# Kernel optimization log

Hardware: AMD Instinct MI355X
Metric: run time of the kernel (lower is better)

Reference implementation:

```python
import jax, jax.numpy as jnp
import numpy as np
from jax import lax

MAX_LEN = 50
MIN_LEN = 5
S = 2 * MAX_LEN + 1  # 101 states (2 branches)
NEG = -10000.0       # score for disallowed transitions


def _build_constraints():
    """Replicates CRFBaseModel.get_crf_constraints(max_len=50, min_len=5, n_branches=2)."""
    pairs = [(0, 0), (0, 1), (MAX_LEN, 1), (MAX_LEN, 0)]
    for i in range(1, MAX_LEN):
        pairs.append((i, i + 1))
        if i > MIN_LEN - 1:
            pairs.append((MIN_LEN - 2, i))
    pairs.append((MAX_LEN - 1, MAX_LEN))
    pairs.append((MAX_LEN - 1, MAX_LEN - 1))
    start_b = 1 + MAX_LEN
    end_b = 2 * MAX_LEN
    pairs += [(0, start_b), (end_b, start_b), (end_b, 0), (end_b, 1), (start_b - 1, start_b)]
    for i in range(start_b, end_b):
        pairs.append((i, i + 1))
        if i > MIN_LEN - 1:
            pairs.append((start_b + MIN_LEN - 3, i))
    pairs.append((end_b - 1, end_b - 1))
    allowed_t = np.zeros((S, S), dtype=bool)
    for (a, c) in pairs:
        allowed_t[a, c] = True
    allowed_s = np.zeros((S,), dtype=bool)
    allowed_s[[0, 1, start_b]] = True
    allowed_e = np.zeros((S,), dtype=bool)
    allowed_e[[0, MAX_LEN, end_b]] = True
    return allowed_t, allowed_s, allowed_e

_ALLOWED_T, _ALLOWED_S, _ALLOWED_E = _build_constraints()


def setup_inputs() -> dict:
    key = jax.random.key(0)
    k0, k1, k2, k3, k4 = jax.random.split(key, 5)
    B, T = 128, 2048
    features = jax.random.normal(k0, (B, T, 64), dtype=jnp.float32)
    mask = jnp.ones((B, T), dtype=bool)
    W = jax.random.normal(k1, (64, 3), dtype=jnp.float32) * 0.05
    b = jnp.zeros((3,), dtype=jnp.float32)
    start_transitions = jax.random.uniform(k2, (S,), minval=-0.1, maxval=0.1, dtype=jnp.float32)
    transitions = jax.random.uniform(k3, (S, S), minval=-0.1, maxval=0.1, dtype=jnp.float32)
    end_transitions = jax.random.uniform(k4, (S,), minval=-0.1, maxval=0.1, dtype=jnp.float32)
    return {"features": features, "mask": mask, "W": W, "b": b,
            "start_transitions": start_transitions, "transitions": transitions,
            "end_transitions": end_transitions}


def reference(features, mask, W, b, start_transitions, transitions, end_transitions):
    B, T, _ = features.shape
    # Apply hand-crafted transition constraints (disallowed -> -10000).
    trans = jnp.where(jnp.asarray(_ALLOWED_T), transitions, NEG)       # [S,S]
    start = jnp.where(jnp.asarray(_ALLOWED_S), start_transitions, NEG)  # [S]
    end = jnp.where(jnp.asarray(_ALLOWED_E), end_transitions, NEG)      # [S]

    # Emissions: linear head to 3 labels, repeated over the state space.
    e3 = features @ W + b  # [B,T,3]
    em = jnp.concatenate([
        e3[..., 0:1],
        jnp.broadcast_to(e3[..., 1:2], (B, T, MAX_LEN)),
        jnp.broadcast_to(e3[..., 2:3], (B, T, MAX_LEN)),
    ], axis=-1)  # [B,T,S]

    eT = jnp.moveaxis(em, 1, 0)    # [T,B,S]
    mT = jnp.moveaxis(mask, 1, 0)  # [T,B]

    # ---- forward (alpha) recursion ----
    a0 = start[None, :] + eT[0]  # [B,S]

    def fwd_step(a, inp):
        e_t, m_t = inp
        a_new = jax.nn.logsumexp(a[:, :, None] + trans[None], axis=1) + e_t
        a = jnp.where(m_t[:, None], a_new, a)
        return a, a

    _, alphas = lax.scan(fwd_step, a0, (eT[1:], mT[1:]))
    alpha = jnp.concatenate([a0[None], alphas], axis=0)  # [T,B,S]
    logZ = jax.nn.logsumexp(alpha[-1] + end[None, :], axis=-1)  # [B]

    # ---- backward (beta) recursion ----
    bT = jnp.broadcast_to(end[None, :], (B, S))

    def bwd_step(b_nxt, inp):
        e_nxt, m_nxt = inp
        b_new = jax.nn.logsumexp(trans[None] + (e_nxt + b_nxt)[:, None, :], axis=2)
        b_nxt = jnp.where(m_nxt[:, None], b_new, b_nxt)
        return b_nxt, b_nxt

    _, betas = lax.scan(bwd_step, bT, (eT[1:], mT[1:]), reverse=True)
    beta = jnp.concatenate([betas, bT[None]], axis=0)  # [T,B,S]

    # marginal probabilities p_t(s) = exp(alpha+beta-logZ) == softmax over states
    probs = jnp.moveaxis(jax.nn.softmax(alpha + beta, axis=-1), 0, 1)  # [B,T,S]

    # ---- Viterbi decode (top_k=1) ----
    def vit_step(v, inp):
        e_t, m_t = inp
        scores = v[:, :, None] + trans[None]   # [B,S_prev,S_cur]
        best = scores.max(axis=1)
        idx = scores.argmax(axis=1).astype(jnp.int32)
        v = jnp.where(m_t[:, None], best + e_t, v)
        return v, idx

    v_last, hist = lax.scan(vit_step, a0, (eT[1:], mT[1:]))  # hist: [T-1,B,S]
    final = v_last + end[None, :]
    last_state = jnp.argmax(final, axis=-1).astype(jnp.int32)  # [B]
    best_score = final.max(axis=-1)

    def back(state, h_t):
        prev = jnp.take_along_axis(h_t, state[:, None], axis=1)[:, 0]
        return prev, prev

    _, prevs = lax.scan(back, last_state, hist, reverse=True)  # [T-1,B]
    paths = jnp.concatenate([prevs, last_state[None]], axis=0).T  # [B,T]
    path_probs = jnp.exp(best_score - logZ)  # [B]
    return probs, paths, path_probs
```

## Files before the change

kernel.cpp:

```cpp
#include <hip/hip_runtime.h>
#include <hip/hip_bf16.h>
#include <math.h>

#define Tn 2048
#define Bn 128
#define Sn 101
#define HP 112
#define CL 128
#define NC (Tn / CL)
#define SEG 256
#define KSEG 8
#define SEGA 128
#define KA 16
#define WWA 128
#define WWARMV 512
#define NEGV -10000.0f
#define DIS  -3.0e38f
#define NINF2 -1.0e30f
#define L2E  1.442695041f

__device__ __forceinline__ int state_label(int s) { return (s == 0) ? 0 : ((s <= 50) ? 1 : 2); }

__device__ __forceinline__ float rl(float v, int lane) {
    return __int_as_float(__builtin_amdgcn_readlane(__float_as_int(v), lane));
}
__device__ __forceinline__ float slog2(float x) {
    return (x > 0.f) ? __log2f(x) : NINF2;
}

__device__ __forceinline__ float dpp_shr1(float x) {
    int xi = __float_as_int(x);
    return __int_as_float(__builtin_amdgcn_update_dpp(xi, xi, 0x138, 0xf, 0xf, false));
}
__device__ __forceinline__ float dpp_shl1(float x) {
    int xi = __float_as_int(x);
    return __int_as_float(__builtin_amdgcn_update_dpp(xi, xi, 0x130, 0xf, 0xf, false));
}
__device__ __forceinline__ float dpp_sum63(float x) {
    x += __int_as_float(__builtin_amdgcn_update_dpp(0, __float_as_int(x), 0x111, 0xf, 0xf, false));
    x += __int_as_float(__builtin_amdgcn_update_dpp(0, __float_as_int(x), 0x112, 0xf, 0xf, false));
    x += __int_as_float(__builtin_amdgcn_update_dpp(0, __float_as_int(x), 0x114, 0xf, 0xf, false));
    x += __int_as_float(__builtin_amdgcn_update_dpp(0, __float_as_int(x), 0x118, 0xf, 0xf, false));
    x += __int_as_float(__builtin_amdgcn_update_dpp(0, __float_as_int(x), 0x142, 0xf, 0xf, false));
    x += __int_as_float(__builtin_amdgcn_update_dpp(0, __float_as_int(x), 0x143, 0xf, 0xf, false));
    return x;
}
__device__ __forceinline__ float dpp_max63(float x) {
// ... 49 lines not shown
    float yA = eA * bA, yB = eB * bB;
    float yAdn = dpp_shl1(yA);
    float y0 = rl(yA, 0), y1 = rl(yB, 0), y51 = rl(yB, 25);
    float c3 = w3A * yA + w3B * yB;
    float c53 = w53A * yA + w53B * yB;
    float s3 = rl(dpp_sum63(c3), 63);
    float s53 = rl(dpp_sum63(c53), 63);
    float chA = (l == 50) ? y51 : yB;
    float nA = wAc * chA + wAs * yA + wA2 * y0 + wA3 * ((l == 0) ? y51 : y1);
    float nB = wBc * yAdn + wBs * yB;
    nB = (l == 1) ? s3 : ((l == 26) ? s53 : nB);
    bA = nA; bB = nB;
}

__global__ __launch_bounds__(256) void k_emis(const float* __restrict__ feat,
                                              const float* __restrict__ W,
                                              const float* __restrict__ bb,
                                              float* __restrict__ e3) {
    int row = blockIdx.x * 256 + threadIdx.x;
    if (row >= Bn * Tn) return;
    const float* f = feat + (size_t)row * 64;
    double a0 = 0.0, a1 = 0.0, a2 = 0.0;
    for (int i = 0; i < 64; i++) {
        double fv = (double)f[i];
        a0 += fv * (double)W[i * 3 + 0];
        a1 += fv * (double)W[i * 3 + 1];
        a2 += fv * (double)W[i * 3 + 2];
    }
    e3[(size_t)row * 3 + 0] = (float)(a0 + (double)bb[0]);
    e3[(size_t)row * 3 + 1] = (float)(a1 + (double)bb[1]);
    e3[(size_t)row * 3 + 2] = (float)(a2 + (double)bb[2]);
}

__global__ __launch_bounds__(64) void k1(const float* __restrict__ e3,
                                         const float* __restrict__ trans,
                                         const float* __restrict__ startT,
                                         const float* __restrict__ endT,
                                         float* __restrict__ alphaOut,
                                         float* __restrict__ shf,
                                         unsigned char* __restrict__ hist,
                                         float* __restrict__ wA,
                                         float* __restrict__ outLast,
                                         float* __restrict__ LSEend,
                                         float* __restrict__ vW,
                                         float* __restrict__ vOut,
                                         float* __restrict__ best,
                                         int* __restrict__ last,
                                         float* __restrict__ bhand)
{
    const int bid = blockIdx.x;
    const int l = threadIdx.x;
    const int sA = 2 * l, sB = 2 * l + 1;
    const bool hA = sA <= 100, hB = sB <= 100;
    const int lblA = state_label(hA ? sA : 100);
    const int lblB = state_label(hB ? sB : 100);

    if (bid < 2048) {
        const int b = bid >> 4, j = bid & 15;
        const size_t ebase = (size_t)b * Tn;
        const int t0 = j * SEGA, t1 = t0 + SEGA;
        int ts = t0 - WWA; if (ts < 0) ts = 0;
        float trAc = (hA && sA >= 1) ? trans[(sA - 1) * Sn + sA] : DIS;
        float trBc = hB ? trans[(sB - 1) * Sn + sB] : DIS;
        float trA1 = (sA >= 5 && sA <= 49) ? trans[3 * Sn + sA] : ((hA && sA <= 1) ? trans[50 * Sn + sA] : DIS);
        float trB1 = (sB >= 5 && sB <= 49) ? trans[3 * Sn + sB] : ((hB && sB <= 1) ? trans[50 * Sn + sB] : DIS);
        float trA2 = ((sA == 51 || sA == 52) || (sA >= 55 && sA <= 99)) ? trans[53 * Sn + sA]
                   : ((hA && sA <= 1) ? trans[100 * Sn + sA] : DIS);
        float trB2 = ((sB == 51 || sB == 52) || (sB >= 55 && sB <= 99)) ? trans[53 * Sn + sB]
                   : ((hB && sB <= 1) ? trans[100 * Sn + sB] : DIS);
        float trA3 = (sA == 0) ? trans[0] : DIS;
        float trB3 = (sB == 49 || sB == 53 || sB == 99) ? trans[sB * Sn + sB] : ((sB == 51) ? trans[0 * Sn + 51] : DIS);
        float trBx = (sB == 51) ? trans[100 * Sn + 51] : DIS;
        float wAc = __expf(trAc), wB0 = __expf(trBc), wA1 = __expf(trA1), wB1 = __expf(trB1);
        float wA2w = __expf(trA2), wB2 = __expf(trB2), wA3w = __expf(trA3), wB3 = __expf(trB3), wBx = __expf(trBx);
        float scA = (sA == 0 || sA == 1 || sA == 51) ? startT[sA] : NEGV;
        float scB = (sB == 1 || sB == 51) ? startT[sB] : NEGV;
        float enA = (sA == 0 || sA == 50 || sA == 100) ? endT[sA] : NEGV;

        float p0, p1, p2, n0 = 0.f, n1 = 0.f, n2 = 0.f;
        int pb = ts + 1;
// ... 1 lines not shown
        p0 = __expf(p0); p1 = __expf(p1); p2 = __expf(p2);

        float aA, aB, sh = 0.f;
        if (ts == 0) {
            float e0A = e3[ebase * 3 + lblA], e0B = e3[ebase * 3 + lblB];
            aA = __expf(scA + e0A);
            aB = __expf(scB + e0B);
            if (j == 0) {
                size_t r = ebase * Sn;
                if (hA) alphaOut[r + sA] = aA;
                if (hB) alphaOut[r + sB] = aB;
                if (l == 0) shf[ebase] = 0.f;
            }
        } else { aA = 1.f; aB = 1.f; }
        int rn = 0;
        int tb = ts + 1;
        for (; tb + 8 <= t0; tb += 8) {
            if ((rn++ & 1) == 0) renorm2(aA, aB, sh);
            if (tb - pb >= 64) { p0 = __expf(n0); p1 = __expf(n1); p2 = __expf(n2); pb += 64; }
            if (tb - pb == 48 && pb + 64 < t1) load_panel(e3, ebase, pb + 64, l, n0, n1, n2);
            #pragma unroll
            for (int v = 0; v < 8; ++v) {
                int t = tb + v;
                float eA, eB;
                panel_sel2(p0, p1, p2, t - pb, l, eA, eB);
                float chA = dpp_shr1(aB);
                float h3 = rl(aB, 1), h53 = rl(aB, 26);
                float a0v = rl(aA, 0), a50v = rl(aA, 25), a100v = rl(aA, 50);
                float s1v = (l == 0) ? a50v : h3;
                float s2v = (l == 0) ? a100v : h53;
                float zA = wAc * chA + wA1 * s1v + wA2w * s2v + wA3w * aA;
                float zB = wB0 * aA + wB1 * s1v + wB2 * s2v + wB3 * ((l == 25) ? a0v : aB) + wBx * a100v;
                aA = zA * eA; aB = zB * eB;
                if (t == t0 - 1 && l == 0) wA[b * KA + j] = slog2(aA) + sh;
            }
        }
        for (; tb < t1; tb += 8) {
            if ((rn++ & 1) == 0) renorm2(aA, aB, sh);
            if (tb - pb >= 64) { p0 = __expf(n0); p1 = __expf(n1); p2 = __expf(n2); pb += 64; }
            if (tb - pb == 48 && pb + 64 < t1) load_panel(e3, ebase, pb + 64, l, n0, n1, n2);
            #pragma unroll
            for (int v = 0; v < 8; ++v) {
                int t = tb + v;
                if (t < t1) {
                    float eA, eB;
                    panel_sel2(p0, p1, p2, t - pb, l, eA, eB);
                    float chA = dpp_shr1(aB);
                    float h3 = rl(aB, 1), h53 = rl(aB, 26);
                    float a0v = rl(aA, 0), a50v = rl(aA, 25), a100v = rl(aA, 50);
                    float s1v = (l == 0) ? a50v : h3;
                    float s2v = (l == 0) ? a100v : h53;
                    float zA = wAc * chA + wA1 * s1v + wA2w * s2v + wA3w * aA;
                    float zB = wB0 * aA + wB1 * s1v + wB2 * s2v + wB3 * ((l == 25) ? a0v : aB) + wBx * a100v;
                    aA = zA * eA; aB = zB * eB;
                    if (t >= t0) {
                        size_t r = (ebase + t) * Sn;
                        if (hA) alphaOut[r + sA] = aA;
                        if (hB) alphaOut[r + sB] = aB;
                        if (l == 0) shf[ebase + t] = sh;
                    }
                    if (t == t0 - 1 && l == 0) wA[b * KA + j] = slog2(aA) + sh;
                }
            }
        }
        if (l == 0) outLast[b * KA + j] = slog2(aA) + sh;
        if (j == KA - 1) {
            float N = lse2_tree(hA ? slog2(aA) + sh + enA * L2E : NINF2,
                                hB ? slog2(aB) + sh + NEGV * L2E : NINF2);
            if (l == 0) LSEend[b] = N;
        }
    } else if (bid < 3072) {
        __builtin_amdgcn_s_setprio(1);
        const int x = bid - 2048;
        const int b = x >> 3, j = x & 7;
        const size_t ebase = (size_t)b * Tn;
        const int t0 = j * SEG, t1 = t0 + SEG;
        int ts = t0 - WWARMV; if (ts < 0) ts = 0;
        float trAc = (hA && sA >= 1) ? trans[(sA - 1) * Sn + sA] : DIS;
        float trBc = hB ? trans[(sB - 1) * Sn + sB] : DIS;
        float trA1 = (sA >= 5 && sA <= 49) ? trans[3 * Sn + sA] : ((hA && sA <= 1) ? trans[50 * Sn + sA] : DIS);
        float trB1 = (sB >= 5 && sB <= 49) ? trans[3 * Sn + sB] : ((hB && sB <= 1) ? trans[50 * Sn + sB] : DIS);
        float trA2 = ((sA == 51 || sA == 52) || (sA >= 55 && sA <= 99)) ? trans[53 * Sn + sA]
                   : ((hA && sA <= 1) ? trans[100 * Sn + sA] : DIS);
        float trB2 = ((sB == 51 || sB == 52) || (sB >= 55 && sB <= 99)) ? trans[53 * Sn + sB]
                   : ((hB && sB <= 1) ? trans[100 * Sn + sB] : DIS);
        float trA3 = (sA == 0) ? trans[0] : DIS;
        float trB3 = (sB == 49 || sB == 53 || sB == 99) ? trans[sB * Sn + sB] : ((sB == 51) ? trans[0 * Sn + 51] : DIS);
        float trBx = (sB == 51) ? trans[100 * Sn + 51] : DIS;
        float scA = (sA == 0 || sA == 1 || sA == 51) ? startT[sA] : NEGV;
        float scB = (sB == 1 || sB == 51) ? startT[sB] : NEGV;
        float enA = (sA == 0 || sA == 50 || sA == 100) ? endT[sA] : NEGV;
        const int idxA1 = (sA <= 1) ? 50 : 3, idxB1 = (sB <= 1) ? 50 : 3;
        const int idxA2 = (sA <= 1) ? 100 : 53, idxB2 = (sB <= 1) ? 100 : 53;
        const int idxB3 = (sB == 51) ? 0 : sB;

        float p0, p1, p2, n0 = 0.f, n1 = 0.f, n2 = 0.f;
        int pb = ts + 1;
        load_panel(e3, ebase, pb, l, p0, p1, p2);

        float vA, vB;
        if (ts == 0) {
            vA = scA + e3[ebase * 3 + lblA];
            vB = scB + e3[ebase * 3 + lblB];
        } else { vA = 0.f; vB = 0.f; }
        size_t hoff = (ebase + (size_t)(t0 > 0 ? t0 - 1 : 0)) * HP + 2 * l;
        int tb = ts + 1;
        for (; tb + 8 <= t0; tb += 8) {
            if (tb - pb >= 64) { p0 = n0; p1 = n1; p2 = n2; pb += 64; }
            if (tb - pb == 48 && pb + 64 < t1) load_panel(e3, ebase, pb + 64, l, n0, n1, n2);
            #pragma unroll
            for (int v = 0; v < 8; ++v) {
                int t = tb + v;
                float eA, eB;
                panel_sel2(p0, p1, p2, t - pb, l, eA, eB);
                float chA = dpp_shr1(vB);
                float h3 = rl(vB, 1), h53 = rl(vB, 26);
                float a0v = rl(vA, 0), a50v = rl(vA, 25), a100v = rl(vA, 50);
                float s1v = (l == 0) ? a50v : h3;
                float s2v = (l == 0) ? a100v : h53;
                float tA0 = chA + trAc, tA1 = s1v + trA1, tA2 = s2v + trA2, tA3 = vA + trA3;
                float tB0 = vA + trBc, tB1 = s1v + trB1, tB2 = s2v + trB2;
                float tB3 = ((l == 25) ? a0v : vB) + trB3;
                float tBx = a100v + trBx;
                float bvA = fmaxf(fmaxf(tA0, tA1), fmaxf(tA2, tA3));
                float bvB = fmaxf(fmaxf(fmaxf(tB0, tB1), fmaxf(tB2, tB3)), tBx);
                if (t == t0 - 1 && l == 0) vW[b * KSEG + j] = bvA + eA;
                vA = bvA + eA;
                vB = bvB + eB;
            }
        }
        for (; tb < t1; tb += 8) {
            if (tb - pb >= 64) { p0 = n0; p1 = n1; p2 = n2; pb += 64; }
            if (tb - pb == 48 && pb + 64 < t1) load_panel(e3, ebase, pb + 64, l, n0, n1, n2);
            #pragma unroll
            for (int v = 0; v < 8; ++v) {
                int t = tb + v;
                if (t < t1) {
                    float eA, eB;
                    panel_sel2(p0, p1, p2, t - pb, l, eA, eB);
                    float chA = dpp_shr1(vB);
                    float h3 = rl(vB, 1), h53 = rl(vB, 26);
                    float a0v = rl(vA, 0), a50v = rl(vA, 25), a100v = rl(vA, 50);
                    float s1v = (l == 0) ? a50v : h3;
                    float s2v = (l == 0) ? a100v : h53;
                    float tA0 = chA + trAc, tA1 = s1v + trA1, tA2 = s2v + trA2, tA3 = vA + trA3;
                    float tB0 = vA + trBc, tB1 = s1v + trB1, tB2 = s2v + trB2;
                    float tB3 = ((l == 25) ? a0v : vB) + trB3;
                    float tBx = a100v + trBx;
                    float bvA = fmaxf(fmaxf(tA0, tA1), fmaxf(tA2, tA3));
                    int biA = min(min((tA0 == bvA) ? (sA - 1) : 127, (tA1 == bvA) ? idxA1 : 127),
                                  min((tA2 == bvA) ? idxA2 : 127, (tA3 == bvA) ? sA : 127));
                    float bvB = fmaxf(fmaxf(fmaxf(tB0, tB1), fmaxf(tB2, tB3)), tBx);
                    int biB = min(min((tB0 == bvB) ? (sB - 1) : 127, (tB1 == bvB) ? idxB1 : 127),
                              min(min((tB2 == bvB) ? idxB2 : 127, (tB3 == bvB) ? idxB3 : 127),
                                  (tBx == bvB) ? 100 : 127));
                    if (t == t0 - 1 && l == 0) vW[b * KSEG + j] = bvA + eA;
                    vA = bvA + eA;
                    vB = bvB + eB;
                    if (t >= t0 && l <= 50) {
                        *reinterpret_cast<unsigned short*>(hist + hoff) =
                            (unsigned short)((biA & 0xff) | ((biB & 0xff) << 8));
                        hoff += HP;
                    }
                }
            }
        }
        if (l == 0) vOut[b * KSEG + j] = vA;
        if (j == KSEG - 1) {
            float fvA = hA ? vA + enA : DIS;
            float fvB = DIS;
            float bv; int bi;
            if (fvA >= fvB) { bv = fvA; bi = sA; } else { bv = fvB; bi = sB; }
            #pragma unroll
            for (int o = 32; o; o >>= 1) {
                float ov = __shfl_xor(bv, o);
                int oi = __shfl_xor(bi, o);
                if (ov > bv || (ov == bv && oi < bi)) { bv = ov; bi = oi; }
            }
            if (l == 0) { best[b] = bv; last[b] = bi; }
        }
    } else {
        const int x = bid - 3072;
        const int b = x >> 4, j = x & 15;
        const size_t ebase = (size_t)b * Tn;
        const int tend = j * SEGA + SEGA;
        int te = tend + WWA; if (te > Tn - 1) te = Tn - 1;
        float trAc = (l < 50) ? trans[sA * Sn + sA + 1] : ((l == 50) ? trans[100 * Sn + 51] : DIS);
        float trBc = (hB && l != 1 && l != 26) ? trans[sB * Sn + sB + 1] : DIS;
        float trAs = (sA == 0) ? trans[0] : DIS;
        float trBs = (sB == 49) ? trans[49 * Sn + 49] : ((sB == 99) ? trans[99 * Sn + 99] : DIS);
        float trA2c = (sA == 50) ? trans[50 * Sn + 0] : ((sA == 100) ? trans[100 * Sn + 0] : DIS);
        float trA3c = (sA == 0) ? trans[0 * Sn + 51]
                    : ((sA == 50) ? trans[50 * Sn + 1] : ((sA == 100) ? trans[100 * Sn + 1] : DIS));
        float tr3A = (sA >= 4 && sA <= 49) ? trans[3 * Sn + sA] : DIS;
        float tr3B = (sB >= 4 && sB <= 49) ? trans[3 * Sn + sB] : DIS;
        float tr53A = (sA >= 51 && sA <= 99) ? trans[53 * Sn + sA] : DIS;
        float tr53B = (sB >= 51 && sB <= 99) ? trans[53 * Sn + sB] : DIS;
        float wAc = __expf(trAc), wBc = __expf(trBc), wAs = __expf(trAs), wBs = __expf(trBs);
        float wA2 = __expf(trA2c), wA3 = __expf(trA3c);
        float w3A = __expf(tr3A), w3B = __expf(tr3B), w53A = __expf(tr53A), w53B = __expf(tr53B);
        float bA, bB, sh = 0.f;
        if (te == Tn - 1) {
            bA = (sA == 0 || sA == 50 || sA == 100) ? __expf(endT[sA]) : 0.f;
            bB = 0.f;
        } else { bA = 1.f; bB = 1.f; }
        if (te > tend) {
            float p0, p1, p2, n0 = 0.f, n1 = 0.f, n2 = 0.f;
            int pb = te - 63;
            load_panel(e3, ebase, pb, l, p0, p1, p2);
            p0 = __expf(p0); p1 = __expf(p1); p2 = __expf(p2);
            int rn = 0;
            for (int tc = te; tc > tend; tc -= 8) {
                if ((rn++ & 1) == 0) renorm2(bA, bB, sh);
                if (tc < pb) { p0 = __expf(n0); p1 = __expf(n1); p2 = __expf(n2); pb -= 64; }
                if (tc - pb == 7 && pb - 1 > tend) load_panel(e3, ebase, pb - 64, l, n0, n1, n2);
                #pragma unroll
                for (int v = 0; v < 8; ++v) {
                    int tcur = tc - v;
                    if (tcur > tend) {
                        float eA, eB;
                        panel_sel2(p0, p1, p2, tcur - pb, l, eA, eB);
                        bwd_lin(eA, eB, bA, bB, wAc, wBc, wAs, wBs, wA2, wA3,
                                w3A, w3B, w53A, w53B, l);
                    }
                }
            }
        }
        float* h0 = bhand + (size_t)(b * KA + j) * 104;
        if (l <= 50) { h0[2 * l] = slog2(bA) + sh; h0[2 * l + 1] = slog2(bB) + sh; }
    }
}

__global__ __launch_bounds__(64) void k2f(const float* __restrict__ e3,
                                          const float* __restrict__ trans,
                                          const float* __restrict__ bhand,
                                          const float* __restrict__ shf,
                                          float* __restrict__ probsIO,
                                          const unsigned char* __restrict__ hist,
                                          unsigned char* __restrict__ M)
{
    __shared__ unsigned char lh[CL * HP];
    if (blockIdx.x >= 2048) {
        int blk = blockIdx.x - 2048; int b = blk >> 4; int c = blk & 15;
        if (c == 0) return;
        const int4* src = (const int4*)(hist + ((size_t)b * Tn + (c * CL - 1)) * HP);
        int4* dst = (int4*)lh;
        for (int i = threadIdx.x; i < CL * HP / 16; i += 64) dst[i] = src[i];
        __syncthreads();
        int cur0 = threadIdx.x;
        int cur1 = threadIdx.x + 64;
        bool h1v = cur1 < Sn;
        if (!h1v) cur1 = 0;
        for (int r = CL - 1; r >= 0; r--) {
            cur0 = lh[r * HP + cur0];
            cur1 = lh[r * HP + cur1];
        }
        M[((size_t)b * NC + c) * HP + threadIdx.x] = (unsigned char)cur0;
        if (h1v) M[((size_t)b * NC + c) * HP + threadIdx.x + 64] = (unsigned char)cur1;
        return;
    }
    const int x = blockIdx.x;
    const int b = x >> 4, j = x & 15;
    const int l = threadIdx.x;
    const int sA = 2 * l, sB = 2 * l + 1;
    const bool hA = sA <= 100, hB = sB <= 100;
    const size_t ebase = (size_t)b * Tn;
    const size_t base = ebase * Sn;
    const int tlo = j * SEGA;
    const int tstart = (j == KA - 1) ? (Tn - 1) : (tlo + SEGA);

    float trAc = (l < 50) ? trans[sA * Sn + sA + 1] : ((l == 50) ? trans[100 * Sn + 51] : DIS);
    float trBc = (hB && l != 1 && l != 26) ? trans[sB * Sn + sB + 1] : DIS;
    float trAs = (sA == 0) ? trans[0] : DIS;
    float trBs = (sB == 49) ? trans[49 * Sn + 49] : ((sB == 99) ? trans[99 * Sn + 99] : DIS);
    float trA2c = (sA == 50) ? trans[50 * Sn + 0] : ((sA == 100) ? trans[100 * Sn + 0] : DIS);
    float trA3c = (sA == 0) ? trans[0 * Sn + 51]
                : ((sA == 50) ? trans[50 * Sn + 1] : ((sA == 100) ? trans[100 * Sn + 1] : DIS));
    float tr3A = (sA >= 4 && sA <= 49) ? trans[3 * Sn + sA] : DIS;
    float tr3B = (sB >= 4 && sB <= 49) ? trans[3 * Sn + sB] : DIS;
    float tr53A = (sA >= 51 && sA <= 99) ? trans[53 * Sn + sA] : DIS;
    float tr53B = (sB >= 51 && sB <= 99) ? trans[53 * Sn + sB] : DIS;
    float wAc = __expf(trAc), wBc = __expf(trBc), wAs = __expf(trAs), wBs = __expf(trBs);
    float wA2 = __expf(trA2c), wA3 = __expf(trA3c);
    float w3A = __expf(tr3A), w3B = __expf(tr3B), w53A = __expf(tr53A), w53B = __expf(tr53B);

    const float* hh = bhand + (size_t)(b * KA + j) * 104;
    float blA = (l <= 50) ? hh[2 * l] : NINF2;
    float blB = (l <= 50) ? hh[2 * l + 1] : NINF2;
    float m = fmaxf(blA, blB);
    #pragma unroll
    for (int o = 32; o; o >>= 1) m = fmaxf(m, __shfl_xor(m, o));
    float sh = m;
    float bA = exp2f(blA - m), bB = exp2f(blB - m);

    float p0, p1, p2, n0 = 0.f, n1 = 0.f, n2 = 0.f;
    int pb = tstart - 63;
    load_panel(e3, ebase, pb, l, p0, p1, p2);
    p0 = __expf(p0); p1 = __expf(p1); p2 = __expf(p2);

    float aRA[8], aRB[8], shR[8];
    #pragma unroll
    for (int u = 0; u < 8; ++u) {
        int ra = tstart - 1 - u; if (ra < 0) ra = 0;
        aRA[u] = probsIO[base + (size_t)ra * Sn + sA];
        aRB[u] = probsIO[base + (size_t)ra * Sn + sB];
        shR[u] = shf[ebase + ra];
    }
    float invS = 1.f, shA0 = 0.f, sh0 = 0.f;
    bool haveN = false;
    if (j == KA - 1) {
        float a0 = probsIO[base + (size_t)(Tn - 1) * Sn + sA];
        float a1 = probsIO[base + (size_t)(Tn - 1) * Sn + sB];
        float shAt = shf[ebase + Tn - 1];
        float prod = (hA ? a0 * bA : 0.f) + (hB ? a1 * bB : 0.f);
        float S = rl(dpp_sum63(prod), 63);
        invS = 1.f / S; shA0 = shAt; sh0 = sh; haveN = true;
        size_t r = base + (size_t)(Tn - 1) * Sn;
        float pA = a0 * bA * invS, pB = a1 * bB * invS;
        if (l < 50) { probsIO[r + sA] = pA; probsIO[r + sB] = pB; }
        else if (l == 50) probsIO[r + sA] = pA;
    }
    int rn = 0;
    for (int tc = tstart; tc > tlo; tc -= 8) {
        if ((rn++ & 1) == 0) renorm2(bA, bB, sh);
        if (tc < pb) { p0 = __expf(n0); p1 = __expf(n1); p2 = __expf(n2); pb -= 64; }
        if (tc - pb == 7 && pb - 1 > tlo) load_panel(e3, ebase, pb - 64, l, n0, n1, n2);
        #pragma unroll
        for (int u = 0; u < 8; ++u) {
            int tcur = tc - u;
            if (tcur > tlo) {
                float eA, eB;
                panel_sel2(p0, p1, p2, tcur - pb, l, eA, eB);
                bwd_lin(eA, eB, bA, bB, wAc, wBc, wAs, wBs, wA2, wA3,
                        w3A, w3B, w53A, w53B, l);
                float aA = aRA[u], aB = aRB[u];
                float shAt = shR[u];
                if (!haveN) {
                    float prod = (hA ? aA * bA : 0.f) + (hB ? aB * bB : 0.f);
                    float S = rl(dpp_sum63(prod), 63);
                    invS = 1.f / S; shA0 = shAt; sh0 = sh; haveN = true;
                }
                float scale = exp2f((shAt - shA0) + (sh - sh0)) * invS;
                size_t r = base + (size_t)(tcur - 1) * Sn;
                float pA = aA * bA * scale, pB = aB * bB * scale;
                if (l < 50) { probsIO[r + sA] = pA; probsIO[r + sB] = pB; }
                else if (l == 50) probsIO[r + sA] = pA;
                int rnx = tcur - 9; if (rnx < 0) rnx = 0;
                aRA[u] = probsIO[base + (size_t)rnx * Sn + sA];
                aRB[u] = probsIO[base + (size_t)rnx * Sn + sB];
                shR[u] = shf[ebase + rnx];
            }
        }
    }
}

__global__ __launch_bounds__(128) void k_chunkC(const unsigned char* __restrict__ hist,
                                                const unsigned char* __restrict__ Mmap,
                                                const int* __restrict__ last,
                                                const float* __restrict__ wA,
                                                const float* __restrict__ outLast,
                                                const float* __restrict__ LSEend,
                                                const float* __restrict__ vW,
                                                const float* __restrict__ vOut,
                                                const float* __restrict__ best,
                                                float* __restrict__ paths,
                                                float* __restrict__ pathp) {
    int blk = blockIdx.x; int b = blk >> 4; int c = blk & 15;
    __shared__ unsigned char lh[(CL - 1) * HP];
    __shared__ unsigned char pl[CL];
    const int4* src = (const int4*)(hist + ((size_t)b * Tn + c * CL) * HP);
    int4* dst = (int4*)lh;
    for (int i = threadIdx.x; i < (CL - 1) * HP / 16; i += 128) dst[i] = src[i];
    if (threadIdx.x == 1 && c == 0) {
        float cA = 0.f, cV = 0.f;
        for (int k = 1; k < KA; ++k) cA += wA[b * KA + k] - outLast[b * KA + k - 1];
        for (int k = 1; k < KSEG; ++k) cV += vOut[b * KSEG + k - 1] - vW[b * KSEG + k];
        float logZ2 = LSEend[b] - cA;
        float bestT = best[b] + cV;
        pathp[b] = exp2f(bestT * L2E - logZ2);
    }
    __syncthreads();
    if (threadIdx.x == 0) {
        int s = last[b];
        for (int cc = NC - 1; cc > c; cc--) s = (int)Mmap[((size_t)b * NC + cc) * HP + s];
        pl[CL - 1] = (unsigned char)s;
        for (int r = CL - 2; r >= 0; r--) { s = lh[r * HP + s]; pl[r] = (unsigned char)s; }
    }
    __syncthreads();
    paths[(size_t)b * Tn + c * CL + threadIdx.x] = (float)pl[threadIdx.x];
}

extern "C" void kernel_launch(void* const* d_in, const int* in_sizes, int n_in,
                              void* d_out, int out_size, void* d_ws, size_t ws_size,
                              hipStream_t stream) {
    const float* feat   = (const float*)d_in[0];
    const float* W      = (const float*)d_in[2];
    const float* bb     = (const float*)d_in[3];
    const float* startT = (const float*)d_in[4];
    const float* trans  = (const float*)d_in[5];
    const float* endT   = (const float*)d_in[6];

    float* out = (float*)d_out;
    float* probs = out;
    float* paths = out + (size_t)Bn * Tn * Sn;
    float* pathp = paths + (size_t)Bn * Tn;

    char* ws = (char*)d_ws;
    size_t off = 0;
    float* e3 = (float*)(ws + off);                    off += (size_t)Bn * Tn * 3 * sizeof(float);
    unsigned char* hist = (unsigned char*)(ws + off);  off += (size_t)Bn * Tn * HP;
    unsigned char* Mmap = (unsigned char*)(ws + off);  off += (size_t)Bn * NC * HP;
    off = (off + 15) & ~(size_t)15;
    float* shf     = (float*)(ws + off); off += (size_t)Bn * Tn * sizeof(float);
    float* wA      = (float*)(ws + off); off += Bn * KA * sizeof(float);
    float* outLast = (float*)(ws + off); off += Bn * KA * sizeof(float);
    float* LSEend  = (float*)(ws + off); off += Bn * sizeof(float);
    float* vW      = (float*)(ws + off); off += Bn * KSEG * sizeof(float);
    float* vOut    = (float*)(ws + off); off += Bn * KSEG * sizeof(float);
    float* best    = (float*)(ws + off); off += Bn * sizeof(float);
    int*   last    = (int*)(ws + off);   off += Bn * sizeof(int);
    off = (off + 15) & ~(size_t)15;
    float* bhand   = (float*)(ws + off); off += (size_t)Bn * KA * 104 * sizeof(float);

    k_emis<<<(Bn * Tn + 255) / 256, 256, 0, stream>>>(feat, W, bb, e3);
    k1<<<5120, 64, 0, stream>>>(e3, trans, startT, endT, probs, shf, hist,
                                wA, outLast, LSEend, vW, vOut, best, last, bhand);
    k2f<<<2048 + Bn * NC, 64, 0, stream>>>(e3, trans, bhand, shf, probs, hist, Mmap);
    k_chunkC<<<Bn * NC, 128, 0, stream>>>(hist, Mmap, last, wA, outLast, LSEend,
                                          vW, vOut, best, paths, pathp);
}
```

Baseline: 263.5 us.

## Move Viterbi forward into backward-marginal kernel and shorten alpha warmup window

The Viterbi max-product forward pass, which writes the backpointer history, moves out of the first kernel into the second kernel, where it runs alongside the backward/marginal blocks. The chunk map composition that used to share the second kernel becomes its own launch, so there are now four kernels. Halving the alpha warmup window from 128 to 64 steps cuts redundant recurrence work per segment, and one wA store inside the warmup loop is dropped as unneeded. The intent is to balance work across launches and shorten the critical path, at the cost of an extra launch and a possible accuracy loss from the shorter warmup.

```diff
diff --git a/kernel.cpp b/kernel.cpp
--- a/kernel.cpp
+++ b/kernel.cpp
@@ -12,7 +12,7 @@
 #define KSEG 8
 #define SEGA 128
 #define KA 16
-#define WWA 128
+#define WWA 64
 #define WWARMV 512
 #define NEGV -10000.0f
 #define DIS  -3.0e38f
@@ -128,20 +128,15 @@
     e3[(size_t)row * 3 + 2] = (float)(a2 + (double)bb[2]);
 }
 
-__global__ __launch_bounds__(64) void k1(const float* __restrict__ e3,
+__global__ __launch_bounds__(64) void kA(const float* __restrict__ e3,
                                          const float* __restrict__ trans,
                                          const float* __restrict__ startT,
                                          const float* __restrict__ endT,
                                          float* __restrict__ alphaOut,
                                          float* __restrict__ shf,
-                                         unsigned char* __restrict__ hist,
                                          float* __restrict__ wA,
                                          float* __restrict__ outLast,
                                          float* __restrict__ LSEend,
-                                         float* __restrict__ vW,
-                                         float* __restrict__ vOut,
-                                         float* __restrict__ best,
-                                         int* __restrict__ last,
                                          float* __restrict__ bhand)
 {
     const int bid = blockIdx.x;
@@ -209,7 +204,6 @@
                 float zA = wAc * chA + wA1 * s1v + wA2w * s2v + wA3w * aA;
                 float zB = wB0 * aA + wB1 * s1v + wB2 * s2v + wB3 * ((l == 25) ? a0v : aB) + wBx * a100v;
                 aA = zA * eA; aB = zB * eB;
-                if (t == t0 - 1 && l == 0) wA[b * KA + j] = slog2(aA) + sh;
             }
         }
         for (; tb < t1; tb += 8) {
@@ -246,118 +240,8 @@
                                 hB ? slog2(aB) + sh + NEGV * L2E : NINF2);
             if (l == 0) LSEend[b] = N;
         }
-    } else if (bid < 3072) {
-        __builtin_amdgcn_s_setprio(1);
+    } else {
         const int x = bid - 2048;
-        const int b = x >> 3, j = x & 7;
-        const size_t ebase = (size_t)b * Tn;
-        const int t0 = j * SEG, t1 = t0 + SEG;
-        int ts = t0 - WWARMV; if (ts < 0) ts = 0;
-        float trAc = (hA && sA >= 1) ? trans[(sA - 1) * Sn + sA] : DIS;
-        float trBc = hB ? trans[(sB - 1) * Sn + sB] : DIS;
-        float trA1 = (sA >= 5 && sA <= 49) ? trans[3 * Sn + sA] : ((hA && sA <= 1) ? trans[50 * Sn + sA] : DIS);
-        float trB1 = (sB >= 5 && sB <= 49) ? trans[3 * Sn + sB] : ((hB && sB <= 1) ? trans[50 * Sn + sB] : DIS);
-        float trA2 = ((sA == 51 || sA == 52) || (sA >= 55 && sA <= 99)) ? trans[53 * Sn + sA]
-                   : ((hA && sA <= 1) ? trans[100 * Sn + sA] : DIS);
-        float trB2 = ((sB == 51 || sB == 52) || (sB >= 55 && sB <= 99)) ? trans[53 * Sn + sB]
-                   : ((hB && sB <= 1) ? trans[100 * Sn + sB] : DIS);
-        float trA3 = (sA == 0) ? trans[0] : DIS;
-        float trB3 = (sB == 49 || sB == 53 || sB == 99) ? trans[sB * Sn + sB] : ((sB == 51) ? trans[0 * Sn + 51] : DIS);
-        float trBx = (sB == 51) ? trans[100 * Sn + 51] : DIS;
-        float scA = (sA == 0 || sA == 1 || sA == 51) ? startT[sA] : NEGV;
-        float scB = (sB == 1 || sB == 51) ? startT[sB] : NEGV;
-        float enA = (sA == 0 || sA == 50 || sA == 100) ? endT[sA] : NEGV;
-        const int idxA1 = (sA <= 1) ? 50 : 3, idxB1 = (sB <= 1) ? 50 : 3;
-        const int idxA2 = (sA <= 1) ? 100 : 53, idxB2 = (sB <= 1) ? 100 : 53;
-        const int idxB3 = (sB == 51) ? 0 : sB;
-
-        float p0, p1, p2, n0 = 0.f, n1 = 0.f, n2 = 0.f;
-        int pb = ts + 1;
-        load_panel(e3, ebase, pb, l, p0, p1, p2);
-
-        float vA, vB;
-        if (ts == 0) {
-            vA = scA + e3[ebase * 3 + lblA];
-            vB = scB + e3[ebase * 3 + lblB];
-        } else { vA = 0.f; vB = 0.f; }
-        size_t hoff = (ebase + (size_t)(t0 > 0 ? t0 - 1 : 0)) * HP + 2 * l;
-        int tb = ts + 1;
-        for (; tb + 8 <= t0; tb += 8) {
-            if (tb - pb >= 64) { p0 = n0; p1 = n1; p2 = n2; pb += 64; }
-            if (tb - pb == 48 && pb + 64 < t1) load_panel(e3, ebase, pb + 64, l, n0, n1, n2);
-            #pragma unroll
-            for (int v = 0; v < 8; ++v) {
-                int t = tb + v;
-                float eA, eB;
-                panel_sel2(p0, p1, p2, t - pb, l, eA, eB);
-                float chA = dpp_shr1(vB);
-                float h3 = rl(vB, 1), h53 = rl(vB, 26);
-                float a0v = rl(vA, 0), a50v = rl(vA, 25), a100v = rl(vA, 50);
-                float s1v = (l == 0) ? a50v : h3;
-                float s2v = (l == 0) ? a100v : h53;
-                float tA0 = chA + trAc, tA1 = s1v + trA1, tA2 = s2v + trA2, tA3 = vA + trA3;
-                float tB0 = vA + trBc, tB1 = s1v + trB1, tB2 = s2v + trB2;
-                float tB3 = ((l == 25) ? a0v : vB) + trB3;
-                float tBx = a100v + trBx;
-                float bvA = fmaxf(fmaxf(tA0, tA1), fmaxf(tA2, tA3));
-                float bvB = fmaxf(fmaxf(fmaxf(tB0, tB1), fmaxf(tB2, tB3)), tBx);
-                if (t == t0 - 1 && l == 0) vW[b * KSEG + j] = bvA + eA;
-                vA = bvA + eA;
-                vB = bvB + eB;
-            }
-        }
-        for (; tb < t1; tb += 8) {
-            if (tb - pb >= 64) { p0 = n0; p1 = n1; p2 = n2; pb += 64; }
-            if (tb - pb == 48 && pb + 64 < t1) load_panel(e3, ebase, pb + 64, l, n0, n1, n2);
-            #pragma unroll
-            for (int v = 0; v < 8; ++v) {
-                int t = tb + v;
-                if (t < t1) {
-                    float eA, eB;
-                    panel_sel2(p0, p1, p2, t - pb, l, eA, eB);
-                    float chA = dpp_shr1(vB);
-                    float h3 = rl(vB, 1), h53 = rl(vB, 26);
-                    float a0v = rl(vA, 0), a50v = rl(vA, 25), a100v = rl(vA, 50);
-                    float s1v = (l == 0) ? a50v : h3;
-                    float s2v = (l == 0) ? a100v : h53;
-                    float tA0 = chA + trAc, tA1 = s1v + trA1, tA2 = s2v + trA2, tA3 = vA + trA3;
-                    float tB0 = vA + trBc, tB1 = s1v + trB1, tB2 = s2v + trB2;
-                    float tB3 = ((l == 25) ? a0v : vB) + trB3;
-                    float tBx = a100v + trBx;
-                    float bvA = fmaxf(fmaxf(tA0, tA1), fmaxf(tA2, tA3));
-                    int biA = min(min((tA0 == bvA) ? (sA - 1) : 127, (tA1 == bvA) ? idxA1 : 127),
-                                  min((tA2 == bvA) ? idxA2 : 127, (tA3 == bvA) ? sA : 127));
-                    float bvB = fmaxf(fmaxf(fmaxf(tB0, tB1), fmaxf(tB2, tB3)), tBx);
-                    int biB = min(min((tB0 == bvB) ? (sB - 1) : 127, (tB1 == bvB) ? idxB1 : 127),
-                              min(min((tB2 == bvB) ? idxB2 : 127, (tB3 == bvB) ? idxB3 : 127),
-                                  (tBx == bvB) ? 100 : 127));
-                    if (t == t0 - 1 && l == 0) vW[b * KSEG + j] = bvA + eA;
-                    vA = bvA + eA;
-                    vB = bvB + eB;
-                    if (t >= t0 && l <= 50) {
-                        *reinterpret_cast<unsigned short*>(hist + hoff) =
-                            (unsigned short)((biA & 0xff) | ((biB & 0xff) << 8));
-                        hoff += HP;
-                    }
-                }
-            }
-        }
-        if (l == 0) vOut[b * KSEG + j] = vA;
-        if (j == KSEG - 1) {
-            float fvA = hA ? vA + enA : DIS;
-            float fvB = DIS;
-            float bv; int bi;
-            if (fvA >= fvB) { bv = fvA; bi = sA; } else { bv = fvB; bi = sB; }
-            #pragma unroll
-            for (int o = 32; o; o >>= 1) {
-                float ov = __shfl_xor(bv, o);
-                int oi = __shfl_xor(bi, o);
-                if (ov > bv || (ov == bv && oi < bi)) { bv = ov; bi = oi; }
-            }
-            if (l == 0) { best[b] = bv; last[b] = bi; }
-        }
-    } else {
-        const int x = bid - 3072;
         const int b = x >> 4, j = x & 15;
         const size_t ebase = (size_t)b * Tn;
         const int tend = j * SEGA + SEGA;
@@ -408,140 +292,261 @@
     }
 }
 
-__global__ __launch_bounds__(64) void k2f(const float* __restrict__ e3,
-                                          const float* __restrict__ trans,
-                                          const float* __restrict__ bhand,
-                                          const float* __restrict__ shf,
-                                          float* __restrict__ probsIO,
-                                          const unsigned char* __restrict__ hist,
-                                          unsigned char* __restrict__ M)
+__global__ __launch_bounds__(64) void kB(const float* __restrict__ e3,
+                                         const float* __restrict__ trans,
+                                         const float* __restrict__ startT,
+                                         const float* __restrict__ endT,
+                                         const float* __restrict__ bhand,
+                                         const float* __restrict__ shf,
+                                         float* __restrict__ probsIO,
+                                         unsigned char* __restrict__ hist,
+                                         float* __restrict__ vW,
+                                         float* __restrict__ vOut,
+                                         float* __restrict__ best,
+                                         int* __restrict__ last)
 {
-    __shared__ unsigned char lh[CL * HP];
-    if (blockIdx.x >= 2048) {
-        int blk = blockIdx.x - 2048; int b = blk >> 4; int c = blk & 15;
-        if (c == 0) return;
-        const int4* src = (const int4*)(hist + ((size_t)b * Tn + (c * CL - 1)) * HP);
-        int4* dst = (int4*)lh;
-        for (int i = threadIdx.x; i < CL * HP / 16; i += 64) dst[i] = src[i];
-        __syncthreads();
-        int cur0 = threadIdx.x;
-        int cur1 = threadIdx.x + 64;
-        bool h1v = cur1 < Sn;
-        if (!h1v) cur1 = 0;
-        for (int r = CL - 1; r >= 0; r--) {
-            cur0 = lh[r * HP + cur0];
-            cur1 = lh[r * HP + cur1];
-        }
-        M[((size_t)b * NC + c) * HP + threadIdx.x] = (unsigned char)cur0;
-        if (h1v) M[((size_t)b * NC + c) * HP + threadIdx.x + 64] = (unsigned char)cur1;
-        return;
-    }
-    const int x = blockIdx.x;
-    const int b = x >> 4, j = x & 15;
+    const int bid = blockIdx.x;
     const int l = threadIdx.x;
     const int sA = 2 * l, sB = 2 * l + 1;
     const bool hA = sA <= 100, hB = sB <= 100;
-    const size_t ebase = (size_t)b * Tn;
-    const size_t base = ebase * Sn;
-    const int tlo = j * SEGA;
-    const int tstart = (j == KA - 1) ? (Tn - 1) : (tlo + SEGA);
-
-    float trAc = (l < 50) ? trans[sA * Sn + sA + 1] : ((l == 50) ? trans[100 * Sn + 51] : DIS);
-    float trBc = (hB && l != 1 && l != 26) ? trans[sB * Sn + sB + 1] : DIS;
-    float trAs = (sA == 0) ? trans[0] : DIS;
-    float trBs = (sB == 49) ? trans[49 * Sn + 49] : ((sB == 99) ? trans[99 * Sn + 99] : DIS);
-    float trA2c = (sA == 50) ? trans[50 * Sn + 0] : ((sA == 100) ? trans[100 * Sn + 0] : DIS);
-    float trA3c = (sA == 0) ? trans[0 * Sn + 51]
-                : ((sA == 50) ? trans[50 * Sn + 1] : ((sA == 100) ? trans[100 * Sn + 1] : DIS));
-    float tr3A = (sA >= 4 && sA <= 49) ? trans[3 * Sn + sA] : DIS;
-    float tr3B = (sB >= 4 && sB <= 49) ? trans[3 * Sn + sB] : DIS;
-    float tr53A = (sA >= 51 && sA <= 99) ? trans[53 * Sn + sA] : DIS;
-    float tr53B = (sB >= 51 && sB <= 99) ? trans[53 * Sn + sB] : DIS;
-    float wAc = __expf(trAc), wBc = __expf(trBc), wAs = __expf(trAs), wBs = __expf(trBs);
-    float wA2 = __expf(trA2c), wA3 = __expf(trA3c);
-    float w3A = __expf(tr3A), w3B = __expf(tr3B), w53A = __expf(tr53A), w53B = __expf(tr53B);
-
-    const float* hh = bhand + (size_t)(b * KA + j) * 104;
-    float blA = (l <= 50) ? hh[2 * l] : NINF2;
-    float blB = (l <= 50) ? hh[2 * l + 1] : NINF2;
-    float m = fmaxf(blA, blB);
-    #pragma unroll
-    for (int o = 32; o; o >>= 1) m = fmaxf(m, __shfl_xor(m, o));
-    float sh = m;
-    float bA = exp2f(blA - m), bB = exp2f(blB - m);
-
-    float p0, p1, p2, n0 = 0.f, n1 = 0.f, n2 = 0.f;
-    int pb = tstart - 63;
-    load_panel(e3, ebase, pb, l, p0, p1, p2);
-    p0 = __expf(p0); p1 = __expf(p1); p2 = __expf(p2);
-
-    float aRA[8], aRB[8], shR[8];
-    #pragma unroll
-    for (int u = 0; u < 8; ++u) {
-        int ra = tstart - 1 - u; if (ra < 0) ra = 0;
-        aRA[u] = probsIO[base + (size_t)ra * Sn + sA];
-        aRB[u] = probsIO[base + (size_t)ra * Sn + sB];
-        shR[u] = shf[ebase + ra];
-    }
-    float invS = 1.f, shA0 = 0.f, sh0 = 0.f;
-    bool haveN = false;
-    if (j == KA - 1) {
-        float a0 = probsIO[base + (size_t)(Tn - 1) * Sn + sA];
-        float a1 = probsIO[base + (size_t)(Tn - 1) * Sn + sB];
-        float shAt = shf[ebase + Tn - 1];
-        float prod = (hA ? a0 * bA : 0.f) + (hB ? a1 * bB : 0.f);
-        float S = rl(dpp_sum63(prod), 63);
-        invS = 1.f / S; shA0 = shAt; sh0 = sh; haveN = true;
-        size_t r = base + (size_t)(Tn - 1) * Sn;
-        float pA = a0 * bA * invS, pB = a1 * bB * invS;
-        if (l < 50) { probsIO[r + sA] = pA; probsIO[r + sB] = pB; }
-        else if (l == 50) probsIO[r + sA] = pA;
-    }
-    int rn = 0;
-    for (int tc = tstart; tc > tlo; tc -= 8) {
-        if ((rn++ & 1) == 0) renorm2(bA, bB, sh);
-        if (tc < pb) { p0 = __expf(n0); p1 = __expf(n1); p2 = __expf(n2); pb -= 64; }
-        if (tc - pb == 7 && pb - 1 > tlo) load_panel(e3, ebase, pb - 64, l, n0, n1, n2);
+    const int lblA = state_label(hA ? sA : 100);
+    const int lblB = state_label(hB ? sB : 100);
+
+    if (bid < 1024) {
+        __builtin_amdgcn_s_setprio(1);
+        const int b = bid >> 3, j = bid & 7;
+        const size_t ebase = (size_t)b * Tn;
+        const int t0 = j * SEG, t1 = t0 + SEG;
+        int ts = t0 - WWARMV; if (ts < 0) ts = 0;
+        float trAc = (hA && sA >= 1) ? trans[(sA - 1) * Sn + sA] : DIS;
+        float trBc = hB ? trans[(sB - 1) * Sn + sB] : DIS;
+        float trA1 = (sA >= 5 && sA <= 49) ? trans[3 * Sn + sA] : ((hA && sA <= 1) ? trans[50 * Sn + sA] : DIS);
+        float trB1 = (sB >= 5 && sB <= 49) ? trans[3 * Sn + sB] : ((hB && sB <= 1) ? trans[50 * Sn + sB] : DIS);
+        float trA2 = ((sA == 51 || sA == 52) || (sA >= 55 && sA <= 99)) ? trans[53 * Sn + sA]
+                   : ((hA && sA <= 1) ? trans[100 * Sn + sA] : DIS);
+        float trB2 = ((sB == 51 || sB == 52) || (sB >= 55 && sB <= 99)) ? trans[53 * Sn + sB]
+                   : ((hB && sB <= 1) ? trans[100 * Sn + sB] : DIS);
+        float trA3 = (sA == 0) ? trans[0] : DIS;
+        float trB3 = (sB == 49 || sB == 53 || sB == 99) ? trans[sB * Sn + sB] : ((sB == 51) ? trans[0 * Sn + 51] : DIS);
+        float trBx = (sB == 51) ? trans[100 * Sn + 51] : DIS;
+        float scA = (sA == 0 || sA == 1 || sA == 51) ? startT[sA] : NEGV;
+        float scB = (sB == 1 || sB == 51) ? startT[sB] : NEGV;
+        float enA = (sA == 0 || sA == 50 || sA == 100) ? endT[sA] : NEGV;
+        const int idxA1 = (sA <= 1) ? 50 : 3, idxB1 = (sB <= 1) ? 50 : 3;
+        const int idxA2 = (sA <= 1) ? 100 : 53, idxB2 = (sB <= 1) ? 100 : 53;
+        const int idxB3 = (sB == 51) ? 0 : sB;
+
+        float p0, p1, p2, n0 = 0.f, n1 = 0.f, n2 = 0.f;
+        int pb = ts + 1;
+        load_panel(e3, ebase, pb, l, p0, p1, p2);
+
+        float vA, vB;
+        if (ts == 0) {
+            vA = scA + e3[ebase * 3 + lblA];
+            vB = scB + e3[ebase * 3 + lblB];
+        } else { vA = 0.f; vB = 0.f; }
+        size_t hoff = (ebase + (size_t)(t0 > 0 ? t0 - 1 : 0)) * HP + 2 * l;
+        int tb = ts + 1;
+        for (; tb + 8 <= t0; tb += 8) {
+            if (tb - pb >= 64) { p0 = n0; p1 = n1; p2 = n2; pb += 64; }
+            if (tb - pb == 48 && pb + 64 < t1) load_panel(e3, ebase, pb + 64, l, n0, n1, n2);
+            #pragma unroll
+            for (int v = 0; v < 8; ++v) {
+                int t = tb + v;
+                float eA, eB;
+                panel_sel2(p0, p1, p2, t - pb, l, eA, eB);
+                float chA = dpp_shr1(vB);
+                float h3 = rl(vB, 1), h53 = rl(vB, 26);
+                float a0v = rl(vA, 0), a50v = rl(vA, 25), a100v = rl(vA, 50);
+                float s1v = (l == 0) ? a50v : h3;
+                float s2v = (l == 0) ? a100v : h53;
+                float tA0 = chA + trAc, tA1 = s1v + trA1, tA2 = s2v + trA2, tA3 = vA + trA3;
+                float tB0 = vA + trBc, tB1 = s1v + trB1, tB2 = s2v + trB2;
+                float tB3 = ((l == 25) ? a0v : vB) + trB3;
+                float tBx = a100v + trBx;
+                float bvA = fmaxf(fmaxf(tA0, tA1), fmaxf(tA2, tA3));
+                float bvB = fmaxf(fmaxf(fmaxf(tB0, tB1), fmaxf(tB2, tB3)), tBx);
+                vA = bvA + eA;
+                vB = bvB + eB;
+            }
+        }
+        for (; tb < t1; tb += 8) {
+            if (tb - pb >= 64) { p0 = n0; p1 = n1; p2 = n2; pb += 64; }
+            if (tb - pb == 48 && pb + 64 < t1) load_panel(e3, ebase, pb + 64, l, n0, n1, n2);
+            #pragma unroll
+            for (int v = 0; v < 8; ++v) {
+                int t = tb + v;
+                if (t < t1) {
+                    float eA, eB;
+                    panel_sel2(p0, p1, p2, t - pb, l, eA, eB);
+                    float chA = dpp_shr1(vB);
+                    float h3 = rl(vB, 1), h53 = rl(vB, 26);
+                    float a0v = rl(vA, 0), a50v = rl(vA, 25), a100v = rl(vA, 50);
+                    float s1v = (l == 0) ? a50v : h3;
+                    float s2v = (l == 0) ? a100v : h53;
+                    float tA0 = chA + trAc, tA1 = s1v + trA1, tA2 = s2v + trA2, tA3 = vA + trA3;
+                    float tB0 = vA + trBc, tB1 = s1v + trB1, tB2 = s2v + trB2;
+                    float tB3 = ((l == 25) ? a0v : vB) + trB3;
+                    float tBx = a100v + trBx;
+                    float bvA = fmaxf(fmaxf(tA0, tA1), fmaxf(tA2, tA3));
+                    int biA = min(min((tA0 == bvA) ? (sA - 1) : 127, (tA1 == bvA) ? idxA1 : 127),
+                                  min((tA2 == bvA) ? idxA2 : 127, (tA3 == bvA) ? sA : 127));
+                    float bvB = fmaxf(fmaxf(fmaxf(tB0, tB1), fmaxf(tB2, tB3)), tBx);
+                    int biB = min(min((tB0 == bvB) ? (sB - 1) : 127, (tB1 == bvB) ? idxB1 : 127),
+                              min(min((tB2 == bvB) ? idxB2 : 127, (tB3 == bvB) ? idxB3 : 127),
+                                  (tBx == bvB) ? 100 : 127));
+                    if (t == t0 - 1 && l == 0) vW[b * KSEG + j] = bvA + eA;
+                    vA = bvA + eA;
+                    vB = bvB + eB;
+                    if (t >= t0 && l <= 50) {
+                        *reinterpret_cast<unsigned short*>(hist + hoff) =
+                            (unsigned short)((biA & 0xff) | ((biB & 0xff) << 8));
+                        hoff += HP;
+                    }
+                }
+            }
+        }
+        if (l == 0) vOut[b * KSEG + j] = vA;
+        if (j == KSEG - 1) {
+            float fvA = hA ? vA + enA : DIS;
+            float fvB = DIS;
+            float bv; int bi;
+            if (fvA >= fvB) { bv = fvA; bi = sA; } else { bv = fvB; bi = sB; }
+            #pragma unroll
+            for (int o = 32; o; o >>= 1) {
+                float ov = __shfl_xor(bv, o);
+                int oi = __shfl_xor(bi, o);
+                if (ov > bv || (ov == bv && oi < bi)) { bv = ov; bi = oi; }
+            }
+            if (l == 0) { best[b] = bv; last[b] = bi; }
+        }
+    } else {
+        const int x = bid - 1024;
+        const int b = x >> 4, j = x & 15;
+        const size_t ebase = (size_t)b * Tn;
+        const size_t base = ebase * Sn;
+        const int tlo = j * SEGA;
+        const int tstart = (j == KA - 1) ? (Tn - 1) : (tlo + SEGA);
+
+        float trAc = (l < 50) ? trans[sA * Sn + sA + 1] : ((l == 50) ? trans[100 * Sn + 51] : DIS);
+        float trBc = (hB && l != 1 && l != 26) ? trans[sB * Sn + sB + 1] : DIS;
+        float trAs = (sA == 0) ? trans[0] : DIS;
+        float trBs = (sB == 49) ? trans[49 * Sn + 49] : ((sB == 99) ? trans[99 * Sn + 99] : DIS);
+        float trA2c = (sA == 50) ? trans[50 * Sn + 0] : ((sA == 100) ? trans[100 * Sn + 0] : DIS);
+        float trA3c = (sA == 0) ? trans[0 * Sn + 51]
+                    : ((sA == 50) ? trans[50 * Sn + 1] : ((sA == 100) ? trans[100 * Sn + 1] : DIS));
+        float tr3A = (sA >= 4 && sA <= 49) ? trans[3 * Sn + sA] : DIS;
+        float tr3B = (sB >= 4 && sB <= 49) ? trans[3 * Sn + sB] : DIS;
+        float tr53A = (sA >= 51 && sA <= 99) ? trans[53 * Sn + sA] : DIS;
+        float tr53B = (sB >= 51 && sB <= 99) ? trans[53 * Sn + sB] : DIS;
+        float wAc = __expf(trAc), wBc = __expf(trBc), wAs = __expf(trAs), wBs = __expf(trBs);
+        float wA2 = __expf(trA2c), wA3 = __expf(trA3c);
+        float w3A = __expf(tr3A), w3B = __expf(tr3B), w53A = __expf(tr53A), w53B = __expf(tr53B);
+
+        const float* hh = bhand + (size_t)(b * KA + j) * 104;
+        float blA = (l <= 50) ? hh[2 * l] : NINF2;
+        float blB = (l <= 50) ? hh[2 * l + 1] : NINF2;
+        float m = fmaxf(blA, blB);
+        #pragma unroll
+        for (int o = 32; o; o >>= 1) m = fmaxf(m, __shfl_xor(m, o));
+        float sh = m;
+        float bA = exp2f(blA - m), bB = exp2f(blB - m);
+
+        float p0, p1, p2, n0 = 0.f, n1 = 0.f, n2 = 0.f;
+        int pb = tstart - 63;
+        load_panel(e3, ebase, pb, l, p0, p1, p2);
+        p0 = __expf(p0); p1 = __expf(p1); p2 = __expf(p2);
+
+        float aRA[8], aRB[8], shR[8];
         #pragma unroll
         for (int u = 0; u < 8; ++u) {
-            int tcur = tc - u;
-            if (tcur > tlo) {
-                float eA, eB;
-                panel_sel2(p0, p1, p2, tcur - pb, l, eA, eB);
-                bwd_lin(eA, eB, bA, bB, wAc, wBc, wAs, wBs, wA2, wA3,
-                        w3A, w3B, w53A, w53B, l);
-                float aA = aRA[u], aB = aRB[u];
-                float shAt = shR[u];
-                if (!haveN) {
-                    float prod = (hA ? aA * bA : 0.f) + (hB ? aB * bB : 0.f);
-                    float S = rl(dpp_sum63(prod), 63);
-                    invS = 1.f / S; shA0 = shAt; sh0 = sh; haveN = true;
+            int ra = tstart - 1 - u; if (ra < 0) ra = 0;
+            aRA[u] = probsIO[base + (size_t)ra * Sn + sA];
+            aRB[u] = probsIO[base + (size_t)ra * Sn + sB];
+            shR[u] = shf[ebase + ra];
+        }
+        float invS = 1.f, shA0 = 0.f, sh0 = 0.f;
+        bool haveN = false;
+        if (j == KA - 1) {
+            float a0 = probsIO[base + (size_t)(Tn - 1) * Sn + sA];
+            float a1 = probsIO[base + (size_t)(Tn - 1) * Sn + sB];
+            float shAt = shf[ebase + Tn - 1];
+            float prod = (hA ? a0 * bA : 0.f) + (hB ? a1 * bB : 0.f);
+            float S = rl(dpp_sum63(prod), 63);
+            invS = 1.f / S; shA0 = shAt; sh0 = sh; haveN = true;
+            size_t r = base + (size_t)(Tn - 1) * Sn;
+            float pA = a0 * bA * invS, pB = a1 * bB * invS;
+            if (l < 50) { probsIO[r + sA] = pA; probsIO[r + sB] = pB; }
+            else if (l == 50) probsIO[r + sA] = pA;
+        }
+        int rn = 0;
+        for (int tc = tstart; tc > tlo; tc -= 8) {
+            if ((rn++ & 1) == 0) renorm2(bA, bB, sh);
+            if (tc < pb) { p0 = __expf(n0); p1 = __expf(n1); p2 = __expf(n2); pb -= 64; }
+            if (tc - pb == 7 && pb - 1 > tlo) load_panel(e3, ebase, pb - 64, l, n0, n1, n2);
+            #pragma unroll
+            for (int u = 0; u < 8; ++u) {
+                int tcur = tc - u;
+                if (tcur > tlo) {
+                    float eA, eB;
+                    panel_sel2(p0, p1, p2, tcur - pb, l, eA, eB);
+                    bwd_lin(eA, eB, bA, bB, wAc, wBc, wAs, wBs, wA2, wA3,
+                            w3A, w3B, w53A, w53B, l);
+                    float aA = aRA[u], aB = aRB[u];
+                    float shAt = shR[u];
+                    if (!haveN) {
+                        float prod = (hA ? aA * bA : 0.f) + (hB ? aB * bB : 0.f);
+                        float S = rl(dpp_sum63(prod), 63);
+                        invS = 1.f / S; shA0 = shAt; sh0 = sh; haveN = true;
+                    }
+                    float scale = exp2f((shAt - shA0) + (sh - sh0)) * invS;
+                    size_t r = base + (size_t)(tcur - 1) * Sn;
+                    float pA = aA * bA * scale, pB = aB * bB * scale;
+                    if (l < 50) { probsIO[r + sA] = pA; probsIO[r + sB] = pB; }
+                    else if (l == 50) probsIO[r + sA] = pA;
+                    int rnx = tcur - 9; if (rnx < 0) rnx = 0;
+                    aRA[u] = probsIO[base + (size_t)rnx * Sn + sA];
+                    aRB[u] = probsIO[base + (size_t)rnx * Sn + sB];
+                    shR[u] = shf[ebase + rnx];
                 }
-                float scale = exp2f((shAt - shA0) + (sh - sh0)) * invS;
-                size_t r = base + (size_t)(tcur - 1) * Sn;
-                float pA = aA * bA * scale, pB = aB * bB * scale;
-                if (l < 50) { probsIO[r + sA] = pA; probsIO[r + sB] = pB; }
-                else if (l == 50) probsIO[r + sA] = pA;
-                int rnx = tcur - 9; if (rnx < 0) rnx = 0;
-                aRA[u] = probsIO[base + (size_t)rnx * Sn + sA];
-                aRB[u] = probsIO[base + (size_t)rnx * Sn + sB];
-                shR[u] = shf[ebase + rnx];
             }
         }
     }
 }
 
-__global__ __launch_bounds__(128) void k_chunkC(const unsigned char* __restrict__ hist,
-                                                const unsigned char* __restrict__ Mmap,
-                                                const int* __restrict__ last,
-                                                const float* __restrict__ wA,
-                                                const float* __restrict__ outLast,
-                                                const float* __restrict__ LSEend,
-                                                const float* __restrict__ vW,
-                                                const float* __restrict__ vOut,
-                                                const float* __restrict__ best,
-                                                float* __restrict__ paths,
-                                                float* __restrict__ pathp) {
+__global__ __launch_bounds__(64) void kC(const unsigned char* __restrict__ hist,
+                                         unsigned char* __restrict__ M)
+{
+    __shared__ unsigned char lh[CL * HP];
+    int blk = blockIdx.x; int b = blk >> 4; int c = blk & 15;
+    if (c == 0) return;
+    const int4* src = (const int4*)(hist + ((size_t)b * Tn + (c * CL - 1)) * HP);
+    int4* dst = (int4*)lh;
+    for (int i = threadIdx.x; i < CL * HP / 16; i += 64) dst[i] = src[i];
+    __syncthreads();
+    int cur0 = threadIdx.x;
+    int cur1 = threadIdx.x + 64;
+    bool h1v = cur1 < Sn;
+    if (!h1v) cur1 = 0;
+    for (int r = CL - 1; r >= 0; r--) {
+        cur0 = lh[r * HP + cur0];
+        cur1 = lh[r * HP + cur1];
+    }
+    M[((size_t)b * NC + c) * HP + threadIdx.x] = (unsigned char)cur0;
+    if (h1v) M[((size_t)b * NC + c) * HP + threadIdx.x + 64] = (unsigned char)cur1;
+}
+
+__global__ __launch_bounds__(128) void kD(const unsigned char* __restrict__ hist,
+                                          const unsigned char* __restrict__ Mmap,
+                                          const int* __restrict__ last,
+                                          const float* __restrict__ wA,
+                                          const float* __restrict__ outLast,
+                                          const float* __restrict__ LSEend,
+                                          const float* __restrict__ vW,
+                                          const float* __restrict__ vOut,
+                                          const float* __restrict__ best,
+                                          float* __restrict__ paths,
+                                          float* __restrict__ pathp) {
     int blk = blockIdx.x; int b = blk >> 4; int c = blk & 15;
     __shared__ unsigned char lh[(CL - 1) * HP];
     __shared__ unsigned char pl[CL];
@@ -600,9 +605,11 @@
     float* bhand   = (float*)(ws + off); off += (size_t)Bn * KA * 104 * sizeof(float);
 
     k_emis<<<(Bn * Tn + 255) / 256, 256, 0, stream>>>(feat, W, bb, e3);
-    k1<<<5120, 64, 0, stream>>>(e3, trans, startT, endT, probs, shf, hist,
-                                wA, outLast, LSEend, vW, vOut, best, last, bhand);
-    k2f<<<2048 + Bn * NC, 64, 0, stream>>>(e3, trans, bhand, shf, probs, hist, Mmap);
-    k_chunkC<<<Bn * NC, 128, 0, stream>>>(hist, Mmap, last, wA, outLast, LSEend,
-                                          vW, vOut, best, paths, pathp);
-}
+    kA<<<4096, 64, 0, stream>>>(e3, trans, startT, endT, probs, shf,
+                                wA, outLast, LSEend, bhand);
+    kB<<<3072, 64, 0, stream>>>(e3, trans, startT, endT, bhand, shf, probs, hist,
+                                vW, vOut, best, last);
+    kC<<<Bn * NC, 64, 0, stream>>>(hist, Mmap);
+    kD<<<Bn * NC, 128, 0, stream>>>(hist, Mmap, last, wA, outLast, LSEend,
+                                    vW, vOut, best, paths, pathp);
+}
```

Result: faster. 229.3 us, median of 2 (-13.0%).
